# Kernel optimization log

Hardware: AMD Instinct MI355X
Metric: run time of the kernel (lower is better)

## Reference

```python
import jax, jax.numpy as jnp
import numpy as np

B, C, H, W = 2, 64, 256, 256
CQ = C // 8    # query/key channels
CR = C // 16   # ShareChannelAttention reduction


def _conv1x1(x, w, b):
    # x: [B,C,H,W], w: [O,C], b: [O]  (1x1 conv == per-pixel linear)
    return jnp.einsum('bchw,oc->bohw', x, w) + b[None, :, None, None]


def _criss_cross(q, k, v):
    # q,k: [B,CQ,H,W], v: [B,C,H,W]; row+column attention with -inf on the
    # H-diagonal, softmax over concatenated H+W energies.
    Hh = q.shape[2]
    eH = jnp.einsum('bchw,bcgw->bhwg', q, k)                 # column (over h') energies
    eH = jnp.where(jnp.eye(Hh, dtype=bool)[:, None, :], -jnp.inf, eH)
    eW = jnp.einsum('bchw,bchv->bhwv', q, k)                 # row (over w') energies
    att = jax.nn.softmax(jnp.concatenate([eH, eW], axis=-1), axis=-1)  # [B,H,W,H+W]
    aH, aW = att[..., :Hh], att[..., Hh:]
    outH = jnp.einsum('bhwg,bcgw->bchw', aH, v)
    outW = jnp.einsum('bhwv,bchv->bchw', aW, v)
    return outH + outW


def _shareca(xa, xb, w1, b1, w2, b2):
    s = xa + xb
    def mlp(p):
        return _conv1x1(jax.nn.relu(_conv1x1(p, w1, b1)), w2, b2)
    gate = jax.nn.sigmoid(mlp(s.mean(axis=(2, 3), keepdims=True)) +
                          mlp(s.max(axis=(2, 3), keepdims=True)))
    return gate * s  # gate*xa + gate*xb


def _bn_relu(x, scale, bias):
    # BatchNorm2d in training mode (batch statistics, biased variance), eps=1e-5
    m = x.mean(axis=(0, 2, 3), keepdims=True)
    v = x.var(axis=(0, 2, 3), keepdims=True)
    xn = (x - m) * jax.lax.rsqrt(v + 1e-5)
    return jax.nn.relu(xn * scale[None, :, None, None] + bias[None, :, None, None])


def setup_inputs() -> dict:
    key = jax.random.key(0)
    ks = jax.random.split(key, 32)
    def n(k, shape, s=0.05):
        return jax.random.normal(k, shape, dtype=jnp.float32) * s
    inp = {
        'x1': n(ks[0], (B, C, H, W), 1.0),
        'x2': n(ks[1], (B, C, H, W), 1.0),
        'wq1': n(ks[2], (CQ, C)), 'bq1': n(ks[3], (CQ,)),
        'wq2': n(ks[4], (CQ, C)), 'bq2': n(ks[5], (CQ,)),
        'wk1': n(ks[6], (CQ, C)), 'bk1': n(ks[7], (CQ,)),
        'wk2': n(ks[8], (CQ, C)), 'bk2': n(ks[9], (CQ,)),
        'wv1': n(ks[10], (C, C)), 'bv1': n(ks[11], (C,)),
        'wv2': n(ks[12], (C, C)), 'bv2': n(ks[13], (C,)),
        'gamma1': n(ks[14], (1,), 0.5), 'gamma2': n(ks[15], (1,), 0.5),
        'sc1_w1': n(ks[16], (CR, C)), 'sc1_b1': n(ks[17], (CR,)),
        'sc1_w2': n(ks[18], (C, CR)), 'sc1_b2': n(ks[19], (C,)),
        'sc2_w1': n(ks[20], (CR, C)), 'sc2_b1': n(ks[21], (CR,)),
        'sc2_w2': n(ks[22], (C, CR)), 'sc2_b2': n(ks[23], (C,)),
        'bn1_scale': jnp.ones((C,), jnp.float32), 'bn1_bias': n(ks[24], (C,)),
        'bn2_scale': jnp.ones((C,), jnp.float32), 'bn2_bias': n(ks[25], (C,)),
    }
    return inp


def reference(x1, x2, wq1, bq1, wq2, bq2, wk1, bk1, wk2, bk2,
              wv1, bv1, wv2, bv2, gamma1, gamma2,
              sc1_w1, sc1_b1, sc1_w2, sc1_b2,
              sc2_w1, sc2_b1, sc2_w2, sc2_b2,
              bn1_scale, bn1_bias, bn2_scale, bn2_bias):
    q1 = _conv1x1(x1, wq1, bq1); q2 = _conv1x1(x2, wq2, bq2)
    k1 = _conv1x1(x1, wk1, bk1); k2 = _conv1x1(x2, wk2, bk2)
    v1 = _conv1x1(x1, wv1, bv1); v2 = _conv1x1(x2, wv2, bv2)
    att1 = _criss_cross(q2, k1, v1)  # out_H_1 + out_W_1
    att2 = _criss_cross(q1, k2, v2)  # out_H_2 + out_W_2
    x_1 = _shareca(gamma2 * att2 + x2, x1, sc1_w1, sc1_b1, sc1_w2, sc1_b2)
    x_2 = _shareca(gamma1 * att1 + x1, x2, sc2_w1, sc2_b1, sc2_w2, sc2_b2)
    out1 = _bn_relu(x_1 + x1, bn1_scale, bn1_bias)
    out2 = _bn_relu(x_2 + x2, bn2_scale, bn2_bias)
    # channel exchange: even channels keep the original input
    mask = (jnp.arange(C) % 2 == 0)[None, :, None, None]
    return jnp.where(mask, x1, out1), jnp.where(mask, x2, out2)
```

## Files before the change

### kernel.cpp

```cpp
#include <hip/hip_runtime.h>
#include <hip/hip_bf16.h>
#include <cstdint>
#include <cstddef>

typedef unsigned short bf16t;
typedef __attribute__((ext_vector_type(8))) short bf16x8;
typedef __attribute__((ext_vector_type(4))) float f32x4;

__device__ __forceinline__ unsigned short f2bf(float f) {
    unsigned u = __float_as_uint(f);
    u += 0x7fffu + ((u >> 16) & 1u);
    return (unsigned short)(u >> 16);
}
__device__ __forceinline__ float bf2f(unsigned short h) {
    return __uint_as_float(((unsigned)h) << 16);
}
__device__ __forceinline__ float bflo(unsigned u) { return __uint_as_float(u << 16); }
__device__ __forceinline__ float bfhi(unsigned u) { return __uint_as_float(u & 0xffff0000u); }
__device__ __forceinline__ unsigned pk2(float a, float b) {
    __hip_bfloat162 h = __float22bfloat162_rn(make_float2(a, b));
    return *(unsigned*)&h;
}
__device__ __forceinline__ bf16x8 mk8(unsigned a, unsigned b, unsigned c, unsigned d) {
    union { uint4 u; bf16x8 v; } cv; cv.u = make_uint4(a, b, c, d); return cv.v;
}

__device__ __forceinline__ unsigned fenc(float f) {
    unsigned u = __float_as_uint(f);
    return (u & 0x80000000u) ? ~u : (u | 0x80000000u);
}
__device__ __forceinline__ float fdec(unsigned u) {
    return __uint_as_float((u & 0x80000000u) ? (u ^ 0x80000000u) : ~u);
}

#define HW 65536

struct ConvArgs {
    const float* x[2];
    const float* wq[2]; const float* bq[2];
    const float* wk[2]; const float* bk[2];
    const float* wv[2]; const float* bv[2];
    bf16t* q[2]; bf16t* k[2]; bf16t* v[2];
    unsigned* zeroR;
};

__global__ __launch_bounds__(256) void conv_qkv(ConvArgs A)
{
    __shared__ __align__(16) bf16t Xlds[256 * 68];

    const int t = threadIdx.x;
    const int z = blockIdx.z;
    const int s = z >> 1, b = z & 1;
    if (z == 0 && blockIdx.x == 0) {
#pragma unroll
        for (int i = 0; i < 6; i++) A.zeroR[t + i * 256] = 0u;
    }
    const int lane = t & 63, wv = t >> 6, quad = lane >> 4, l16 = lane & 15;
    const int px0 = blockIdx.x * 256;

    const float* xp = A.x[s] + (size_t)b * 64 * HW + px0 + t;
    {
        unsigned xw[32];
#pragma unroll
        for (int c = 0; c < 32; c++)
            xw[c] = pk2(xp[(size_t)(2 * c) * HW], xp[(size_t)(2 * c + 1) * HW]);
#pragma unroll
        for (int g = 0; g < 16; g++)
            *(uint2*)&Xlds[t * 68 + g * 4] = make_uint2(xw[2 * g], xw[2 * g + 1]);
    }

    bf16x8 bfr[5][2];
    float bo[5];
    bf16t* obase[5];
#pragma unroll
    for (int ot = 0; ot < 5; ot++) {
        const int o = ot * 16 + l16;
        const float* wrow;
        if (o < 8)       { wrow = A.wq[s] + o * 64;        bo[ot] = A.bq[s][o];
                           obase[ot] = A.q[s] + (size_t)(b * 8 + o) * HW; }
        else if (o < 16) { wrow = A.wk[s] + (o - 8) * 64;  bo[ot] = A.bk[s][o - 8];
                           obase[ot] = A.k[s] + (size_t)(b * 8 + o - 8) * HW; }
        else             { wrow = A.wv[s] + (o - 16) * 64; bo[ot] = A.bv[s][o - 16];
                           obase[ot] = A.v[s] + (size_t)(b * 64 + o - 16) * HW; }
#pragma unroll
        for (int ks = 0; ks < 2; ks++) {
            const float* wp = wrow + ks * 32 + quad * 8;
            bfr[ot][ks] = mk8(pk2(wp[0], wp[1]), pk2(wp[2], wp[3]),
                              pk2(wp[4], wp[5]), pk2(wp[6], wp[7]));
        }
    }

    __syncthreads();

    bf16x8 afr[4][2];
#pragma unroll
    for (int i = 0; i < 4; i++)
#pragma unroll
        for (int ks = 0; ks < 2; ks++) {
            const int base = (wv * 64 + i * 16 + l16) * 68 + ks * 32 + quad * 8;
            const uint2 lo = *(const uint2*)&Xlds[base];
            const uint2 hi = *(const uint2*)&Xlds[base + 4];
            afr[i][ks] = mk8(lo.x, lo.y, hi.x, hi.y);
        }

    const f32x4 z4 = {0.f, 0.f, 0.f, 0.f};
    f32x4 acc[4][5];
#pragma unroll
    for (int i = 0; i < 4; i++)
#pragma unroll
        for (int ot = 0; ot < 5; ot++) acc[i][ot] = z4;

#pragma unroll
    for (int ks = 0; ks < 2; ks++)
#pragma unroll
        for (int i = 0; i < 4; i++)
#pragma unroll
            for (int ot = 0; ot < 5; ot++)
                acc[i][ot] = __builtin_amdgcn_mfma_f32_16x16x32_bf16(afr[i][ks], bfr[ot][ks], acc[i][ot], 0, 0, 0);

#pragma unroll
    for (int i = 0; i < 4; i++) {
        const int px = px0 + wv * 64 + i * 16 + quad * 4;
#pragma unroll
        for (int ot = 0; ot < 5; ot++) {
            uint2 u;
            u.x = pk2(acc[i][ot][0] + bo[ot], acc[i][ot][1] + bo[ot]);
            u.y = pk2(acc[i][ot][2] + bo[ot], acc[i][ot][3] + bo[ot]);
            *(uint2*)&obase[ot][px] = u;
        }
    }
}

__global__ __launch_bounds__(256) void transpose16(const bf16t* __restrict__ in, bf16t* __restrict__ out)
{
    __shared__ bf16t tile[64][68];
    const size_t zo = (size_t)blockIdx.z * HW;
    const int i0 = blockIdx.y * 64, j0 = blockIdx.x * 64;
    const int lc = threadIdx.x & 63, rg = threadIdx.x >> 6;
#pragma unroll
    for (int rr = 0; rr < 16; rr++) {
        int row = rg * 16 + rr;
        tile[row][lc] = in[zo + (size_t)(i0 + row) * 256 + j0 + lc];
    }
    __syncthreads();
#pragma unroll
    for (int rr = 0; rr < 16; rr++) {
        int row = rg * 16 + rr;
        out[zo + (size_t)(j0 + row) * 256 + i0 + lc] = tile[lc][row];
    }
}

struct RowccArgs {
    const bf16t* q[4]; const bf16t* k[4]; const bf16t* v[4];
    bf16t* o[4]; float* so[4];
};

__global__ __launch_bounds__(256, 3) void rowcc_mfma(RowccArgs P)
{
    __shared__ __align__(16) char smem[54272];
    bf16t* vs = (bf16t*)smem;
    bf16t* ps = (bf16t*)(smem + 33792);

    const int t = threadIdx.x;
    const int r = blockIdx.x, b = blockIdx.y, z = blockIdx.z;
    const bool mask = (z < 2);
    const int lane = t & 63, wv = t >> 6, quad = lane >> 4, l16 = lane & 15;
    const int wband = wv * 64;

    const bf16t* qp = P.q[z];
    const bf16t* kp = P.k[z];
    const bf16t* vp = P.v[z];

    const size_t vb = (size_t)b * 64 * HW + (size_t)r * 256;
#pragma unroll
    for (int i = 0; i < 8; i++) {
        const int qd = i * 256 + t;
        const int c = qd >> 5, jc = (qd & 31) * 8;
        *(uint4*)&vs[c * 264 + jc] = *(const uint4*)&vp[vb + (size_t)c * HW + jc];
    }

    const bf16x8 zfr = {0, 0, 0, 0, 0, 0, 0, 0};
    bf16x8 qfr[4] = {zfr, zfr, zfr, zfr};
    const size_t rowb = (size_t)b * 8 * HW + (size_t)r * 256;
    if (quad == 0) {
#pragma unroll
        for (int wt = 0; wt < 4; wt++) {
            const int w_g = wband + wt * 16 + l16;
#pragma unroll
            for (int ch = 0; ch < 8; ch++)
                qfr[wt][ch] = (short)qp[rowb + (size_t)ch * HW + w_g];
        }
    }

    const f32x4 z4 = {0.f, 0.f, 0.f, 0.f};
    f32x4 acc[4][4];
#pragma unroll
    for (int i = 0; i < 4; i++)
#pragma unroll
        for (int j = 0; j < 4; j++) acc[i][j] = z4;
    float s_t[4] = {0.f, 0.f, 0.f, 0.f};

    bf16x8 kcur[2] = {zfr, zfr};
    if (quad == 0) {
#pragma unroll
        for (int jtile = 0; jtile < 2; jtile++)
#pragma unroll
            for (int ch = 0; ch < 8; ch++)
                kcur[jtile][ch] = (short)kp[rowb + (size_t)ch * HW + jtile * 16 + l16];
    }

    __syncthreads();

    for (int jt = 0; jt < 8; jt++) {
        const int j0 = jt * 32;
        f32x4 e[4][2];
#pragma unroll
        for (int wt = 0; wt < 4; wt++)
#pragma unroll
            for (int jtile = 0; jtile < 2; jtile++)
                e[wt][jtile] = __builtin_amdgcn_mfma_f32_16x16x32_bf16(kcur[jtile], qfr[wt], z4, 0, 0, 0);

        bf16x8 knext[2] = {zfr, zfr};
        if (jt < 7 && quad == 0) {
            const int jn = (jt + 1) * 32;
#pragma unroll
            for (int jtile = 0; jtile < 2; jtile++)
#pragma unroll
                for (int ch = 0; ch < 8; ch++)
                    knext[jtile][ch] = (short)kp[rowb + (size_t)ch * HW + jn + jtile * 16 + l16];
        }

        if (mask && (jt >> 1) == wv) {
#pragma unroll
            for (int wt = 0; wt < 4; wt++) {
                const int w_g = wband + wt * 16 + l16;
#pragma unroll
                for (int jtile = 0; jtile < 2; jtile++)
#pragma unroll
                    for (int rr = 0; rr < 4; rr++)
                        if (j0 + jtile * 16 + quad * 4 + rr == w_g) e[wt][jtile][rr] = -3.0e38f;
            }
        }

#pragma unroll
        for (int wt = 0; wt < 4; wt++) {
#pragma unroll
            for (int jtile = 0; jtile < 2; jtile++) {
                const float p0 = __expf(e[wt][jtile][0]);
                const float p1 = __expf(e[wt][jtile][1]);
                const float p2 = __expf(e[wt][jtile][2]);
                const float p3 = __expf(e[wt][jtile][3]);
                s_t[wt] += (p0 + p1) + (p2 + p3);
                uint2 u; u.x = pk2(p0, p1); u.y = pk2(p2, p3);
                *(uint2*)&ps[(wband + wt * 16 + l16) * 40 + jtile * 16 + quad * 4] = u;
            }
        }

        bf16x8 afr[4], bfr[4];
#pragma unroll
        for (int wt = 0; wt < 4; wt++)
            afr[wt] = *(const bf16x8*)&ps[(wband + wt * 16 + l16) * 40 + quad * 8];
#pragma unroll
        for (int ct = 0; ct < 4; ct++)
            bfr[ct] = *(const bf16x8*)&vs[(ct * 16 + l16) * 264 + j0 + quad * 8];
#pragma unroll
        for (int wt = 0; wt < 4; wt++)
#pragma unroll
            for (int ct = 0; ct < 4; ct++)
                acc[wt][ct] = __builtin_amdgcn_mfma_f32_16x16x32_bf16(afr[wt], bfr[ct], acc[wt][ct], 0, 0, 0);

        kcur[0] = knext[0]; kcur[1] = knext[1];
    }

#pragma unroll
    for (int wt = 0; wt < 4; wt++) {
        float s = s_t[wt];
        s += __shfl_xor(s, 16, 64);
        s += __shfl_xor(s, 32, 64);
        s_t[wt] = s;
    }
    if (quad == 0) {
#pragma unroll
        for (int wt = 0; wt < 4; wt++) {
            const int w_g = wband + wt * 16 + l16;
            if (mask)
                P.so[z][(size_t)b * HW + w_g * 256 + r] = s_t[wt];
            else
                P.so[z][(size_t)b * HW + r * 256 + w_g] = s_t[wt];
        }
    }

    __syncthreads();
    bf16t* o_lds = (bf16t*)smem;
#pragma unroll
    for (int wt = 0; wt < 4; wt++) {
        const int w0 = wband + wt * 16 + quad * 4;
#pragma unroll
        for (int ct = 0; ct < 4; ct++) {
            const int c = ct * 16 + l16;
            uint2 u;
            u.x = pk2(acc[wt][ct][0], acc[wt][ct][1]);
            u.y = pk2(acc[wt][ct][2], acc[wt][ct][3]);
            *(uint2*)&o_lds[c * 264 + w0] = u;
        }
    }
    __syncthreads();
    bf16t* ob = P.o[z] + (size_t)b * 64 * HW + (size_t)r * 256;
#pragma unroll
    for (int i = 0; i < 8; i++) {
        const int qd = i * 256 + t;
        const int c = qd >> 5, w8 = (qd & 31) * 8;
        *(uint4*)&ob[(size_t)c * HW + w8] = *(const uint4*)&o_lds[c * 264 + w8];
    }
}

__global__ __launch_bounds__(256) void combine_reduce(
    const bf16t* __restrict__ oH1, const bf16t* __restrict__ oW1,
    const bf16t* __restrict__ oH2, const bf16t* __restrict__ oW2,
    const float* __restrict__ sH1, const float* __restrict__ sW1,
    const float* __restrict__ sH2, const float* __restrict__ sW2,
    const float* __restrict__ x1, const float* __restrict__ x2,
    const float* __restrict__ gamma1, const float* __restrict__ gamma2,
    bf16t* __restrict__ s1, bf16t* __restrict__ s2,
    float* __restrict__ accum, unsigned* __restrict__ accmax)
{
    const int t = threadIdx.x, chunk = blockIdx.x, c = blockIdx.y, b = blockIdx.z;
    const float g1v = gamma1[0], g2v = gamma2[0];
    const size_t cb = ((size_t)(b * 64 + c)) * HW;
    const size_t pb = (size_t)b * HW;

    float pS1 = 0, pSS1 = 0, pSX1 = 0, pX1 = 0, pXX1 = 0, pM1 = -3e38f;
    float pS2 = 0, pSS2 = 0, pSX2 = 0, pX2 = 0, pXX2 = 0, pM2 = -3e38f;

    for (int i = 0; i < 16; i++) {
        const int pidx = chunk * 4096 + i * 256 + t;
        const float inv1 = 1.f / (sH1[pb + pidx] + sW1[pb + pidx]);
        const float inv2 = 1.f / (sH2[pb + pidx] + sW2[pb + pidx]);
        const float a1 = (bf2f(oH1[cb + pidx]) + bf2f(oW1[cb + pidx])) * inv1;
        const float a2 = (bf2f(oH2[cb + pidx]) + bf2f(oW2[cb + pidx])) * inv2;
        const float x1v = x1[cb + pidx], x2v = x2[cb + pidx];
        const float s1v = g2v * a2 + x2v + x1v;
        const float s2v = g1v * a1 + x1v + x2v;
        s1[cb + pidx] = f2bf(s1v);
        s2[cb + pidx] = f2bf(s2v);
        pS1 += s1v; pSS1 += s1v * s1v; pSX1 += s1v * x1v; pX1 += x1v; pXX1 += x1v * x1v; pM1 = fmaxf(pM1, s1v);
        pS2 += s2v; pSS2 += s2v * s2v; pSX2 += s2v * x2v; pX2 += x2v; pXX2 += x2v * x2v; pM2 = fmaxf(pM2, s2v);
    }

    __shared__ float wred[12][4];
    float vals[12] = {pS1, pSS1, pSX1, pX1, pXX1, pM1, pS2, pSS2, pSX2, pX2, pXX2, pM2};
    const int lane = t & 63, wave = t >> 6;
#pragma unroll
    for (int iv = 0; iv < 12; iv++) {
        float v = vals[iv];
        const bool isMax = (iv == 5 || iv == 11);
#pragma unroll
        for (int off = 32; off > 0; off >>= 1) {
            const float o = __shfl_down(v, off, 64);
            v = isMax ? fmaxf(v, o) : (v + o);
        }
        if (lane == 0) wred[iv][wave] = v;
    }
    __syncthreads();
    if (t < 12) {
        const bool isMax = (t == 5 || t == 11);
        float v = wred[t][0];
        for (int i = 1; i < 4; i++) v = isMax ? fmaxf(v, wred[t][i]) : (v + wred[t][i]);
        const int stream = (t >= 6) ? 1 : 0;
        const int kk = t - stream * 6;
        if (kk == 5) atomicMax(&accmax[(stream * 2 + b) * 64 + c], fenc(v));
        else atomicAdd(&accum[((stream * 2 + b) * 64 + c) * 5 + kk], v);
    }
}

__global__ __launch_bounds__(256) void gates_bn(
    const float* __restrict__ accum, const unsigned* __restrict__ accmax,
    const float* __restrict__ sc1_w1, const float* __restrict__ sc1_b1,
    const float* __restrict__ sc1_w2, const float* __restrict__ sc1_b2,
    const float* __restrict__ sc2_w1, const float* __restrict__ sc2_b1,
    const float* __restrict__ sc2_w2, const float* __restrict__ sc2_b2,
    const float* __restrict__ bn1_scale, const float* __restrict__ bn1_bias,
    const float* __restrict__ bn2_scale, const float* __restrict__ bn2_bias,
    float* __restrict__ gates, float* __restrict__ AB)
{
    const int t = threadIdx.x;
    const int stream = t >> 7, b = (t >> 6) & 1, c = t & 63;
    __shared__ float meanS[256], maxS[256], e1S[256], e2S[256];

    const float S = accum[t * 5 + 0], SS = accum[t * 5 + 1], SX = accum[t * 5 + 2];
    const float X = accum[t * 5 + 3], XX = accum[t * 5 + 4];
    meanS[t] = S * (1.f / 65536.f);
    maxS[t] = fdec(accmax[t]);
    __syncthreads();

    const float* w1 = stream ? sc2_w1 : sc1_w1;
    const float* b1 = stream ? sc2_b1 : sc1_b1;
    const float* w2 = stream ? sc2_w2 : sc1_w2;
    const float* b2 = stream ? sc2_b2 : sc1_b2;
    float om = b2[c], ox = b2[c];
    const int base = stream * 128 + b * 64;
#pragma unroll
    for (int r = 0; r < 4; r++) {
        float hm = b1[r], hx = b1[r];
        for (int cc = 0; cc < 64; cc++) {
            hm += w1[r * 64 + cc] * meanS[base + cc];
            hx += w1[r * 64 + cc] * maxS[base + cc];
        }
        hm = fmaxf(hm, 0.f); hx = fmaxf(hx, 0.f);
        om += w2[c * 4 + r] * hm;
        ox += w2[c * 4 + r] * hx;
    }
    const float gate = 1.f / (1.f + __expf(-(om + ox)));
    gates[t] = gate;
    e1S[t] = gate * S + X;
    e2S[t] = gate * gate * SS + 2.f * gate * SX + XX;
    __syncthreads();
    if (b == 0) {
        const float sumY = e1S[t] + e1S[t + 64];
        const float sumY2 = e2S[t] + e2S[t + 64];
        const float meanY = sumY * (1.f / 131072.f);
        const float varY = sumY2 * (1.f / 131072.f) - meanY * meanY;
        const float sc = stream ? bn2_scale[c] : bn1_scale[c];
        const float bi = stream ? bn2_bias[c] : bn1_bias[c];
        const float A = sc * rsqrtf(varY + 1e-5f);
        AB[stream * 128 + c] = A;
        AB[stream * 128 + 64 + c] = bi - meanY * A;
    }
}

__global__ __launch_bounds__(256) void finalize(
    const bf16t* __restrict__ s1, const bf16t* __restrict__ s2,
    const float* __restrict__ x1, const float* __restrict__ x2,
    const float* __restrict__ gates, const float* __restrict__ AB,
    float* __restrict__ out)
{
    const size_t tid = (size_t)blockIdx.x * 256 + threadIdx.x;
    const size_t idx = tid * 4;
    const int b = (int)(idx >> 22);
    const int c = (int)((idx >> 16) & 63);
    const bool odd = (c & 1) != 0;
    const float g1 = gates[b * 64 + c], g2 = gates[128 + b * 64 + c];
    const float A1 = AB[c], B1 = AB[64 + c], A2 = AB[128 + c], B2 = AB[192 + c];

    const uint2 su1 = *(const uint2*)(s1 + idx);
    const uint2 su2 = *(const uint2*)(s2 + idx);
    const float4 x1v = *(const float4*)(x1 + idx);
    const float4 x2v = *(const float4*)(x2 + idx);
    float s1f[4] = {bflo(su1.x), bfhi(su1.x), bflo(su1.y), bfhi(su1.y)};
    float s2f[4] = {bflo(su2.x), bfhi(su2.x), bflo(su2.y), bfhi(su2.y)};
    float xa[4] = {x1v.x, x1v.y, x1v.z, x1v.w};
    float xb[4] = {x2v.x, x2v.y, x2v.z, x2v.w};
    float o1[4], o2[4];
#pragma unroll
    for (int j = 0; j < 4; j++) {
        const float y1 = g1 * s1f[j] + xa[j];
        const float y2 = g2 * s2f[j] + xb[j];
        o1[j] = odd ? fmaxf(A1 * y1 + B1, 0.f) : xa[j];
        o2[j] = odd ? fmaxf(A2 * y2 + B2, 0.f) : xb[j];
    }
    *(float4*)(out + idx) = make_float4(o1[0], o1[1], o1[2], o1[3]);
    *(float4*)(out + 8388608 + idx) = make_float4(o2[0], o2[1], o2[2], o2[3]);
}

extern "C" void kernel_launch(void* const* d_in, const int* in_sizes, int n_in,
                              void* d_out, int out_size, void* d_ws, size_t ws_size,
                              hipStream_t stream) {
    (void)in_sizes; (void)n_in; (void)out_size; (void)ws_size;
    const float* x1 = (const float*)d_in[0];
    const float* x2 = (const float*)d_in[1];
    const float* wq1 = (const float*)d_in[2];  const float* bq1 = (const float*)d_in[3];
    const float* wq2 = (const float*)d_in[4];  const float* bq2 = (const float*)d_in[5];
    const float* wk1 = (const float*)d_in[6];  const float* bk1 = (const float*)d_in[7];
    const float* wk2 = (const float*)d_in[8];  const float* bk2 = (const float*)d_in[9];
    const float* wv1 = (const float*)d_in[10]; const float* bv1 = (const float*)d_in[11];
    const float* wv2 = (const float*)d_in[12]; const float* bv2 = (const float*)d_in[13];
    const float* gamma1 = (const float*)d_in[14];
    const float* gamma2 = (const float*)d_in[15];
    const float* sc1_w1 = (const float*)d_in[16]; const float* sc1_b1 = (const float*)d_in[17];
    const float* sc1_w2 = (const float*)d_in[18]; const float* sc1_b2 = (const float*)d_in[19];
    const float* sc2_w1 = (const float*)d_in[20]; const float* sc2_b1 = (const float*)d_in[21];
    const float* sc2_w2 = (const float*)d_in[22]; const float* sc2_b2 = (const float*)d_in[23];
    const float* bn1_scale = (const float*)d_in[24]; const float* bn1_bias = (const float*)d_in[25];
    const float* bn2_scale = (const float*)d_in[26]; const float* bn2_bias = (const float*)d_in[27];

    char* p = (char*)d_ws;
    const size_t SZ_QK = 2097152;
    const size_t SZ_V = 16777216;
    const size_t SZ_ST = 524288;

    bf16t* q1 = (bf16t*)(p + 0 * SZ_QK);
    bf16t* k1 = (bf16t*)(p + 1 * SZ_QK);
    bf16t* q2 = (bf16t*)(p + 2 * SZ_QK);
    bf16t* k2 = (bf16t*)(p + 3 * SZ_QK);
    bf16t* v1 = (bf16t*)(p + 4 * SZ_QK);
    bf16t* v2 = (bf16t*)(p + 4 * SZ_QK + SZ_V);
    size_t off = 4 * SZ_QK + 2 * SZ_V;
    bf16t* q1T = (bf16t*)(p + off + 0 * SZ_QK);
    bf16t* k1T = (bf16t*)(p + off + 1 * SZ_QK);
    bf16t* q2T = (bf16t*)(p + off + 2 * SZ_QK);
    bf16t* k2T = (bf16t*)(p + off + 3 * SZ_QK);
    bf16t* v1T = (bf16t*)(p + off + 4 * SZ_QK);
    bf16t* v2T = (bf16t*)(p + off + 4 * SZ_QK + SZ_V);
    off += 4 * SZ_QK + 2 * SZ_V;
    bf16t* oH1T = (bf16t*)(p + off); off += SZ_V;
    bf16t* oH2T = (bf16t*)(p + off); off += SZ_V;
    bf16t* oW1 = (bf16t*)(p + off); off += SZ_V;
    bf16t* oW2 = (bf16t*)(p + off); off += SZ_V;
    float* sH1 = (float*)(p + off); off += SZ_ST;
    float* sH2 = (float*)(p + off); off += SZ_ST;
    float* sW1 = (float*)(p + off); off += SZ_ST;
    float* sW2 = (float*)(p + off); off += SZ_ST;
    float* accum = (float*)(p + off);
    unsigned* accmax = (unsigned*)(p + off + 5120);
    float* gates = (float*)(p + off + 6144);
    float* AB = (float*)(p + off + 7168);

    bf16t* oH1 = v1T;
    bf16t* oH2 = v2T;
    bf16t* s1 = oH1T;
    bf16t* s2 = oH2T;

    ConvArgs CA;
    CA.x[0] = x1; CA.x[1] = x2;
    CA.wq[0] = wq1; CA.wq[1] = wq2; CA.bq[0] = bq1; CA.bq[1] = bq2;
    CA.wk[0] = wk1; CA.wk[1] = wk2; CA.bk[0] = bk1; CA.bk[1] = bk2;
    CA.wv[0] = wv1; CA.wv[1] = wv2; CA.bv[0] = bv1; CA.bv[1] = bv2;
    CA.q[0] = q1; CA.q[1] = q2; CA.k[0] = k1; CA.k[1] = k2;
    CA.v[0] = v1; CA.v[1] = v2;
    CA.zeroR = (unsigned*)accum;
    conv_qkv<<<dim3(256, 1, 4), 256, 0, stream>>>(CA);

    transpose16<<<dim3(4, 4, 320), 256, 0, stream>>>(q1, q1T);

    RowccArgs RA;
    RA.q[0] = q2T; RA.k[0] = k1T; RA.v[0] = v1T; RA.o[0] = oH1T; RA.so[0] = sH1;
    RA.q[1] = q1T; RA.k[1] = k2T; RA.v[1] = v2T; RA.o[1] = oH2T; RA.so[1] = sH2;
    RA.q[2] = q2;  RA.k[2] = k1;  RA.v[2] = v1;  RA.o[2] = oW1;  RA.so[2] = sW1;
    RA.q[3] = q1;  RA.k[3] = k2;  RA.v[3] = v2;  RA.o[3] = oW2;  RA.so[3] = sW2;
    rowcc_mfma<<<dim3(256, 2, 4), 256, 0, stream>>>(RA);

    transpose16<<<dim3(4, 4, 256), 256, 0, stream>>>(oH1T, oH1);

    combine_reduce<<<dim3(16, 64, 2), 256, 0, stream>>>(
        oH1, oW1, oH2, oW2, sH1, sW1, sH2, sW2, x1, x2, gamma1, gamma2,
        s1, s2, accum, accmax);

    gates_bn<<<1, 256, 0, stream>>>(accum, accmax,
                                    sc1_w1, sc1_b1, sc1_w2, sc1_b2,
                                    sc2_w1, sc2_b1, sc2_w2, sc2_b2,
                                    bn1_scale, bn1_bias, bn2_scale, bn2_bias,
                                    gates, AB);

    finalize<<<8192, 256, 0, stream>>>(s1, s2, x1, x2, gates, AB, (float*)d_out);
}
```

Measured before the change: 328.6 us.

## Keep softmax probabilities in registers and skip even-channel intermediate traffic

The attention kernel now permutes the key column order so each lane's exp'd energy outputs already form the A-operand fragment for the P·V MFMA. This removes the LDS staging buffer for probabilities and the write/read round trip, shrinks shared memory, and raises the occupancy hint from 3 to 4 blocks. The combine kernel stops writing s1/s2 for even channels, and finalize skips loading them along with gates and BN coefficients there, since those outputs are just copies of the input. The risk is higher register pressure under the tighter launch bound.

```diff
diff --git a/kernel.cpp b/kernel.cpp
--- a/kernel.cpp
+++ b/kernel.cpp
@@ -155,17 +155,16 @@
     bf16t* o[4]; float* so[4];
 };
 
-__global__ __launch_bounds__(256, 3) void rowcc_mfma(RowccArgs P)
+__global__ __launch_bounds__(256, 4) void rowcc_mfma(RowccArgs P)
 {
-    __shared__ __align__(16) char smem[54272];
-    bf16t* vs = (bf16t*)smem;
-    bf16t* ps = (bf16t*)(smem + 33792);
+    __shared__ __align__(16) bf16t vs[64 * 264];
 
     const int t = threadIdx.x;
     const int r = blockIdx.x, b = blockIdx.y, z = blockIdx.z;
     const bool mask = (z < 2);
     const int lane = t & 63, wv = t >> 6, quad = lane >> 4, l16 = lane & 15;
     const int wband = wv * 64;
+    const int jperm = 8 * (l16 >> 2) + (l16 & 3);
 
     const bf16t* qp = P.q[z];
     const bf16t* kp = P.k[z];
@@ -206,19 +205,18 @@
         for (int jtile = 0; jtile < 2; jtile++)
 #pragma unroll
             for (int ch = 0; ch < 8; ch++)
-                kcur[jtile][ch] = (short)kp[rowb + (size_t)ch * HW + jtile * 16 + l16];
+                kcur[jtile][ch] = (short)kp[rowb + (size_t)ch * HW + jtile * 4 + jperm];
     }
 
     __syncthreads();
 
     for (int jt = 0; jt < 8; jt++) {
         const int j0 = jt * 32;
-        f32x4 e[4][2];
-#pragma unroll
-        for (int wt = 0; wt < 4; wt++)
-#pragma unroll
-            for (int jtile = 0; jtile < 2; jtile++)
-                e[wt][jtile] = __builtin_amdgcn_mfma_f32_16x16x32_bf16(kcur[jtile], qfr[wt], z4, 0, 0, 0);
+
+        bf16x8 bfr[4];
+#pragma unroll
+        for (int ct = 0; ct < 4; ct++)
+            bfr[ct] = *(const bf16x8*)&vs[(ct * 16 + l16) * 264 + j0 + quad * 8];
 
         bf16x8 knext[2] = {zfr, zfr};
         if (jt < 7 && quad == 0) {
@@ -227,47 +225,40 @@
             for (int jtile = 0; jtile < 2; jtile++)
 #pragma unroll
                 for (int ch = 0; ch < 8; ch++)
-                    knext[jtile][ch] = (short)kp[rowb + (size_t)ch * HW + jn + jtile * 16 + l16];
-        }
-
-        if (mask && (jt >> 1) == wv) {
-#pragma unroll
-            for (int wt = 0; wt < 4; wt++) {
+                    knext[jtile][ch] = (short)kp[rowb + (size_t)ch * HW + jn + jtile * 4 + jperm];
+        }
+
+        const bool dodiag = mask && ((jt >> 1) == wv);
+
+#pragma unroll
+        for (int wt = 0; wt < 4; wt++) {
+            f32x4 e0 = __builtin_amdgcn_mfma_f32_16x16x32_bf16(kcur[0], qfr[wt], z4, 0, 0, 0);
+            f32x4 e1 = __builtin_amdgcn_mfma_f32_16x16x32_bf16(kcur[1], qfr[wt], z4, 0, 0, 0);
+
+            if (dodiag) {
                 const int w_g = wband + wt * 16 + l16;
-#pragma unroll
-                for (int jtile = 0; jtile < 2; jtile++)
-#pragma unroll
-                    for (int rr = 0; rr < 4; rr++)
-                        if (j0 + jtile * 16 + quad * 4 + rr == w_g) e[wt][jtile][rr] = -3.0e38f;
+                const int jb = j0 + 8 * quad;
+#pragma unroll
+                for (int rr = 0; rr < 4; rr++) {
+                    if (jb + rr == w_g)     e0[rr] = -3.0e38f;
+                    if (jb + 4 + rr == w_g) e1[rr] = -3.0e38f;
+                }
             }
-        }
-
-#pragma unroll
-        for (int wt = 0; wt < 4; wt++) {
-#pragma unroll
-            for (int jtile = 0; jtile < 2; jtile++) {
-                const float p0 = __expf(e[wt][jtile][0]);
-                const float p1 = __expf(e[wt][jtile][1]);
-                const float p2 = __expf(e[wt][jtile][2]);
-                const float p3 = __expf(e[wt][jtile][3]);
-                s_t[wt] += (p0 + p1) + (p2 + p3);
-                uint2 u; u.x = pk2(p0, p1); u.y = pk2(p2, p3);
-                *(uint2*)&ps[(wband + wt * 16 + l16) * 40 + jtile * 16 + quad * 4] = u;
+
+            float p[8];
+#pragma unroll
+            for (int rr = 0; rr < 4; rr++) {
+                p[rr]     = __expf(e0[rr]);
+                p[4 + rr] = __expf(e1[rr]);
             }
-        }
-
-        bf16x8 afr[4], bfr[4];
-#pragma unroll
-        for (int wt = 0; wt < 4; wt++)
-            afr[wt] = *(const bf16x8*)&ps[(wband + wt * 16 + l16) * 40 + quad * 8];
-#pragma unroll
-        for (int ct = 0; ct < 4; ct++)
-            bfr[ct] = *(const bf16x8*)&vs[(ct * 16 + l16) * 264 + j0 + quad * 8];
-#pragma unroll
-        for (int wt = 0; wt < 4; wt++)
+            s_t[wt] += ((p[0] + p[1]) + (p[2] + p[3])) + ((p[4] + p[5]) + (p[6] + p[7]));
+            const bf16x8 pa = mk8(pk2(p[0], p[1]), pk2(p[2], p[3]),
+                                  pk2(p[4], p[5]), pk2(p[6], p[7]));
+
 #pragma unroll
             for (int ct = 0; ct < 4; ct++)
-                acc[wt][ct] = __builtin_amdgcn_mfma_f32_16x16x32_bf16(afr[wt], bfr[ct], acc[wt][ct], 0, 0, 0);
+                acc[wt][ct] = __builtin_amdgcn_mfma_f32_16x16x32_bf16(pa, bfr[ct], acc[wt][ct], 0, 0, 0);
+        }
 
         kcur[0] = knext[0]; kcur[1] = knext[1];
     }
@@ -291,7 +282,7 @@
     }
 
     __syncthreads();
-    bf16t* o_lds = (bf16t*)smem;
+    bf16t* o_lds = vs;
 #pragma unroll
     for (int wt = 0; wt < 4; wt++) {
         const int w0 = wband + wt * 16 + quad * 4;
@@ -328,6 +319,7 @@
     const float g1v = gamma1[0], g2v = gamma2[0];
     const size_t cb = ((size_t)(b * 64 + c)) * HW;
     const size_t pb = (size_t)b * HW;
+    const bool codd = (c & 1) != 0;
 
     float pS1 = 0, pSS1 = 0, pSX1 = 0, pX1 = 0, pXX1 = 0, pM1 = -3e38f;
     float pS2 = 0, pSS2 = 0, pSX2 = 0, pX2 = 0, pXX2 = 0, pM2 = -3e38f;
@@ -341,8 +333,10 @@
         const float x1v = x1[cb + pidx], x2v = x2[cb + pidx];
         const float s1v = g2v * a2 + x2v + x1v;
         const float s2v = g1v * a1 + x1v + x2v;
-        s1[cb + pidx] = f2bf(s1v);
-        s2[cb + pidx] = f2bf(s2v);
+        if (codd) {
+            s1[cb + pidx] = f2bf(s1v);
+            s2[cb + pidx] = f2bf(s2v);
+        }
         pS1 += s1v; pSS1 += s1v * s1v; pSX1 += s1v * x1v; pX1 += x1v; pXX1 += x1v * x1v; pM1 = fmaxf(pM1, s1v);
         pS2 += s2v; pSS2 += s2v * s2v; pSX2 += s2v * x2v; pX2 += x2v; pXX2 += x2v * x2v; pM2 = fmaxf(pM2, s2v);
     }
@@ -439,24 +433,30 @@
     const int b = (int)(idx >> 22);
     const int c = (int)((idx >> 16) & 63);
     const bool odd = (c & 1) != 0;
-    const float g1 = gates[b * 64 + c], g2 = gates[128 + b * 64 + c];
-    const float A1 = AB[c], B1 = AB[64 + c], A2 = AB[128 + c], B2 = AB[192 + c];
-
-    const uint2 su1 = *(const uint2*)(s1 + idx);
-    const uint2 su2 = *(const uint2*)(s2 + idx);
+
     const float4 x1v = *(const float4*)(x1 + idx);
     const float4 x2v = *(const float4*)(x2 + idx);
-    float s1f[4] = {bflo(su1.x), bfhi(su1.x), bflo(su1.y), bfhi(su1.y)};
-    float s2f[4] = {bflo(su2.x), bfhi(su2.x), bflo(su2.y), bfhi(su2.y)};
     float xa[4] = {x1v.x, x1v.y, x1v.z, x1v.w};
     float xb[4] = {x2v.x, x2v.y, x2v.z, x2v.w};
     float o1[4], o2[4];
-#pragma unroll
-    for (int j = 0; j < 4; j++) {
-        const float y1 = g1 * s1f[j] + xa[j];
-        const float y2 = g2 * s2f[j] + xb[j];
-        o1[j] = odd ? fmaxf(A1 * y1 + B1, 0.f) : xa[j];
-        o2[j] = odd ? fmaxf(A2 * y2 + B2, 0.f) : xb[j];
+
+    if (odd) {
+        const float g1 = gates[b * 64 + c], g2 = gates[128 + b * 64 + c];
+        const float A1 = AB[c], B1 = AB[64 + c], A2 = AB[128 + c], B2 = AB[192 + c];
+        const uint2 su1 = *(const uint2*)(s1 + idx);
+        const uint2 su2 = *(const uint2*)(s2 + idx);
+        float s1f[4] = {bflo(su1.x), bfhi(su1.x), bflo(su1.y), bfhi(su1.y)};
+        float s2f[4] = {bflo(su2.x), bfhi(su2.x), bflo(su2.y), bfhi(su2.y)};
+#pragma unroll
+        for (int j = 0; j < 4; j++) {
+            const float y1 = g1 * s1f[j] + xa[j];
+            const float y2 = g2 * s2f[j] + xb[j];
+            o1[j] = fmaxf(A1 * y1 + B1, 0.f);
+            o2[j] = fmaxf(A2 * y2 + B2, 0.f);
+        }
+    } else {
+#pragma unroll
+        for (int j = 0; j < 4; j++) { o1[j] = xa[j]; o2[j] = xb[j]; }
     }
     *(float4*)(out + idx) = make_float4(o1[0], o1[1], o1[2], o1[3]);
     *(float4*)(out + 8388608 + idx) = make_float4(o2[0], o2[1], o2[2], o2[3]);
```

After: 382.0 us. +16.3%, slower.
